# Optimization experiments

Hardware: AMD Instinct MI355X
Metric: run time of the kernel (lower is better)

The kernel has to match this reference:

```python
import jax, jax.numpy as jnp
import numpy as np

B, T, V, E, H = 2048, 80, 80, 8, 256  # batch, seq_len, vocab/num_classes, embed_dim, n_hidden
FORGET_BIAS = 1.0  # TF BasicLSTMCell default


def setup_inputs() -> dict:
    key = jax.random.key(0)
    ks = jax.random.split(key, 8)
    return {
        "features": jax.random.randint(ks[0], (B, T), 0, V, dtype=jnp.int32),
        "embedding": jax.random.normal(ks[1], (V, E), dtype=jnp.float32) * 0.1,
        "W1": jax.random.normal(ks[2], (E + H, 4 * H), dtype=jnp.float32) * 0.05,
        "b1": jnp.zeros((4 * H,), jnp.float32),
        "W2": jax.random.normal(ks[3], (H + H, 4 * H), dtype=jnp.float32) * 0.05,
        "b2": jnp.zeros((4 * H,), jnp.float32),
        "Wd": jax.random.normal(ks[4], (H, V), dtype=jnp.float32) * 0.05,
        "bd": jnp.zeros((V,), jnp.float32),
    }


def _lstm_layer(x, W, b):
    # x: [B, T, in]; TF BasicLSTMCell gate order: i, j(cell cand), f, o
    h_dim = W.shape[1] // 4

    def step(carry, xt):
        c, h = carry
        z = jnp.concatenate([xt, h], axis=-1) @ W + b  # [B, 4H]
        i, j, f, o = jnp.split(z, 4, axis=-1)
        c = c * jax.nn.sigmoid(f + FORGET_BIAS) + jax.nn.sigmoid(i) * jnp.tanh(j)
        h = jnp.tanh(c) * jax.nn.sigmoid(o)
        return (c, h), h

    b_dim = x.shape[0]
    init = (jnp.zeros((b_dim, h_dim), x.dtype), jnp.zeros((b_dim, h_dim), x.dtype))
    _, hs = jax.lax.scan(step, init, jnp.swapaxes(x, 0, 1))  # hs: [T, B, H]
    return jnp.swapaxes(hs, 0, 1)  # [B, T, H]


def reference(features, embedding, W1, b1, W2, b2, Wd, bd):
    x = embedding[features]            # [B, T, E] embedding lookup
    h1 = _lstm_layer(x, W1, b1)        # [B, T, H]
    h2 = _lstm_layer(h1, W2, b2)       # [B, T, H]
    logits = h2[:, -1, :] @ Wd + bd    # dense on last timestep -> [B, V]
    return logits
```

## Files before the change

### kernel.cpp

```cpp
#include <hip/hip_runtime.h>
#include <hip/hip_bf16.h>


#define BB 2048
#define TT 80
#define VV 80
#define HH 256

typedef _Float16 half8 __attribute__((ext_vector_type(8)));
typedef _Float16 half4v __attribute__((ext_vector_type(4)));
typedef float f32x4 __attribute__((ext_vector_type(4)));

__device__ __forceinline__ float sigf(float x) { return 1.0f / (1.0f + __expf(-x)); }
__device__ __forceinline__ float tanhfast(float x) { return 2.0f * sigf(2.0f * x) - 1.0f; }

__device__ __forceinline__ int swz(int row, int kbyte) {
    return row * 512 + (kbyte ^ ((row & 7) << 4));
}

__global__ void prep_table(const float* __restrict__ emb, const float* __restrict__ W1,
                           const float* __restrict__ b1, float* __restrict__ tbl) {
    int v = blockIdx.x, d = threadIdx.x;
    float4 s;
    s.x = b1[d]; s.y = b1[256 + d]; s.z = b1[512 + d] + 1.0f; s.w = b1[768 + d];
    #pragma unroll
    for (int e = 0; e < 8; ++e) {
        float xv = emb[v * 8 + e];
        const float* wr = W1 + (size_t)e * 1024;
        s.x = fmaf(xv, wr[d], s.x);
        s.y = fmaf(xv, wr[256 + d], s.y);
        s.z = fmaf(xv, wr[512 + d], s.z);
        s.w = fmaf(xv, wr[768 + d], s.w);
    }
    ((float4*)tbl)[v * 256 + d] = s;
}

__global__ void prep_w1_v2(const float* __restrict__ W1, _Float16* __restrict__ Wf) {
    int tid = blockIdx.x * 256 + threadIdx.x;
    int l = tid & 63, g = (tid >> 6) & 3, kk = (tid >> 8) & 7, w = (tid >> 11) & 15;
    int col = g * 256 + w * 16 + (l & 15);
    size_t base = ((size_t)((w * 8 + kk) * 4 + g) * 64 + l) * 8;
    #pragma unroll
    for (int e = 0; e < 8; ++e) {
        int krow = 8 + kk * 32 + (l >> 4) * 8 + e;
        Wf[base + e] = (_Float16)W1[(size_t)krow * 1024 + col];
    }
}
__global__ void prep_w2h_v2(const float* __restrict__ W2, _Float16* __restrict__ Wf) {
    int tid = blockIdx.x * 256 + threadIdx.x;
    int l = tid & 63, g = (tid >> 6) & 3, kk = (tid >> 8) & 7, w = (tid >> 11) & 15;
    int col = g * 256 + w * 16 + (l & 15);
    size_t base = ((size_t)((w * 8 + kk) * 4 + g) * 64 + l) * 8;
    #pragma unroll
    for (int e = 0; e < 8; ++e) {
        int krow = 256 + kk * 32 + (l >> 4) * 8 + e;
        Wf[base + e] = (_Float16)W2[(size_t)krow * 1024 + col];
    }
}
__global__ void prep_w2za_v2(const float* __restrict__ W2, _Float16* __restrict__ Wf) {
    int tid = blockIdx.x * 256 + threadIdx.x;
    int l = tid & 63, g = (tid >> 6) & 3, kk = (tid >> 8) & 7, w = (tid >> 11) & 15;
    int col = g * 256 + w * 16 + (l & 15);
    size_t base = ((size_t)((w * 8 + kk) * 4 + g) * 64 + l) * 8;
    #pragma unroll
    for (int e = 0; e < 8; ++e) {
        int krow = kk * 32 + (l >> 4) * 8 + e;
        Wf[base + e] = (_Float16)W2[(size_t)krow * 1024 + col];
    }
}
__global__ void prep_w2_old(const float* __restrict__ W2, _Float16* __restrict__ Wf) {
    int tid = blockIdx.x * 256 + threadIdx.x;
    int l = tid & 63, kk = (tid >> 6) & 7, j = (tid >> 9) & 1;
    int g = (tid >> 10) & 3, s = (tid >> 12) & 1, w = tid >> 13;
    int col = g * 256 + w * 32 + j * 16 + (l & 15);
    size_t base = ((size_t)((w * 16 + s * 8 + g * 2 + j) * 8 + kk) * 64 + l) * 8;
    #pragma unroll
    for (int e = 0; e < 8; ++e) {
        int krow = (1 - s) * 256 + kk * 32 + (l >> 4) * 8 + e;
        Wf[base + e] = (_Float16)W2[(size_t)krow * 1024 + col];
    }
}

__global__ __launch_bounds__(1024) void lstm1_v3(
    const int* __restrict__ feats, const float* __restrict__ tbl,
    const _Float16* __restrict__ Wf, _Float16* __restrict__ h1out)
{
    __shared__ char hb0[8192], hb1[8192];
    __shared__ int f_lds[16 * TT];
    const int tid = threadIdx.x, l = tid & 63, w = tid >> 6;
    const int row_a = l & 15, chunk = l >> 4;
    const int dim = w * 16 + (l & 15);
    const int crow0 = (l >> 4) * 4;
    const int brow = blockIdx.x * 16;

    for (int i = tid; i < 2048; i += 1024) ((float*)hb0)[i] = 0.f;
    for (int i = tid; i < 16 * TT; i += 1024)
        f_lds[i] = feats[(size_t)(brow + i / TT) * TT + (i % TT)];
    float c[4] = {};
    const float4* tblv = (const float4*)tbl;
    const half8* wp = (const half8*)Wf + (size_t)w * 2048;
    __syncthreads();

    for (int t = 0; t < TT; ++t) {
        char* cur = (t & 1) ? hb1 : hb0;
        char* nxt = (t & 1) ? hb0 : hb1;

        float4 tb[4];
        #pragma unroll
        for (int m = 0; m < 4; ++m) {
            int f = f_lds[(crow0 + m) * TT + t];
            tb[m] = tblv[f * 256 + dim];
        }

        f32x4 acc[4];
        #pragma unroll
        for (int g = 0; g < 4; ++g) acc[g] = (f32x4){0.f, 0.f, 0.f, 0.f};

        half8 wbuf[3][4];
        #pragma unroll
        for (int p = 0; p < 3; ++p)
            #pragma unroll
            for (int g = 0; g < 4; ++g) wbuf[p][g] = wp[(size_t)(p * 4 + g) * 64 + l];
        half8 aA = *(const half8*)(cur + swz(row_a, 0 * 64 + chunk * 16));
        half8 aB = *(const half8*)(cur + swz(row_a, 1 * 64 + chunk * 16));

        #pragma unroll
        for (int kk = 0; kk < 8; ++kk) {
            half8 av = (kk & 1) ? aB : aA;
            #pragma unroll
            for (int g = 0; g < 4; ++g)
                acc[g] = __builtin_amdgcn_mfma_f32_16x16x32_f16(
                    av, wbuf[kk % 3][g], acc[g], 0, 0, 0);
            if (kk + 2 < 8) {
                half8 an = *(const half8*)(cur + swz(row_a, (kk + 2) * 64 + chunk * 16));
                if (kk & 1) aB = an; else aA = an;
            }
            if (kk + 3 < 8) {
                #pragma unroll
                for (int g = 0; g < 4; ++g)
                    wbuf[(kk + 3) % 3][g] = wp[(size_t)((kk + 3) * 4 + g) * 64 + l];
            }
        }

        #pragma unroll
        for (int m = 0; m < 4; ++m) {
            const int R = crow0 + m;
            float zi = acc[0][m] + tb[m].x, zj = acc[1][m] + tb[m].y;
            float zf = acc[2][m] + tb[m].z, zo = acc[3][m] + tb[m].w;
            c[m] = c[m] * sigf(zf) + sigf(zi) * tanhfast(zj);
            float hv = tanhfast(c[m]) * sigf(zo);
            *(_Float16*)(nxt + swz(R, dim * 2)) = (_Float16)hv;
            h1out[((size_t)t * BB + brow + R) * HH + dim] = (_Float16)hv;
        }
        __syncthreads();
    }
}

__global__ __launch_bounds__(1024) void za_gemm_v3(
    const _Float16* __restrict__ h1, const _Float16* __restrict__ Wz,
    _Float16* __restrict__ za, int t0)
{
    const int tid = threadIdx.x, l = tid & 63, w = tid >> 6;
    const int chunk = l >> 4;
    const int dim = w * 16 + (l & 15);
    const size_t rloc = (size_t)blockIdx.x * 16;
    const size_t rglob = (size_t)t0 * BB + rloc;

    half8 a[8];
    #pragma unroll
    for (int kk = 0; kk < 8; ++kk)
        a[kk] = *(const half8*)(h1 + (rglob + (l & 15)) * HH + kk * 32 + chunk * 8);

    f32x4 acc[4];
    #pragma unroll
    for (int g = 0; g < 4; ++g) acc[g] = (f32x4){0.f, 0.f, 0.f, 0.f};
    const half8* wp = (const half8*)Wz + (size_t)w * 2048;
    half8 wbuf[2][4];
    #pragma unroll
    for (int g = 0; g < 4; ++g) wbuf[0][g] = wp[g * 64 + l];
    #pragma unroll
    for (int kk = 0; kk < 8; ++kk) {
        const int cur = kk & 1;
        if (kk < 7) {
            #pragma unroll
            for (int g = 0; g < 4; ++g)
                wbuf[cur ^ 1][g] = wp[(size_t)((kk + 1) * 4 + g) * 64 + l];
        }
        #pragma unroll
        for (int g = 0; g < 4; ++g)
            acc[g] = __builtin_amdgcn_mfma_f32_16x16x32_f16(
                a[kk], wbuf[cur][g], acc[g], 0, 0, 0);
    }
    #pragma unroll
    for (int m = 0; m < 4; ++m) {
        half4v v = { (_Float16)acc[0][m], (_Float16)acc[1][m],
                     (_Float16)acc[2][m], (_Float16)acc[3][m] };
        *(half4v*)(za + (rloc + chunk * 4 + m) * 1024 + dim * 4) = v;
    }
}

__global__ __launch_bounds__(1024) void lstm2_v3(
    const _Float16* __restrict__ za, const _Float16* __restrict__ Wf,
    const float* __restrict__ b2, float* __restrict__ c_state,
    _Float16* __restrict__ h_state, const float* __restrict__ Wd,
    const float* __restrict__ bd, float* __restrict__ out,
    int t0, int tc, int last)
{
    __shared__ char hb0[8192], hb1[8192];
    const int tid = threadIdx.x, l = tid & 63, w = tid >> 6;
    const int row_a = l & 15, chunk = l >> 4;
    const int dim = w * 16 + (l & 15);
    const int crow0 = (l >> 4) * 4;
    const int brow = blockIdx.x * 16;

    float bv[4];
    #pragma unroll
    for (int g = 0; g < 4; ++g) bv[g] = b2[g * 256 + dim] + (g == 2 ? 1.0f : 0.0f);

    float c[4];
    if (t0 == 0) {
        for (int i = tid; i < 2048; i += 1024) ((float*)hb0)[i] = 0.f;
        #pragma unroll
        for (int m = 0; m < 4; ++m) c[m] = 0.f;
    } else {
        for (int i = tid; i < 4096; i += 1024) {
            int r = i >> 8, d = i & 255;
            *(_Float16*)(hb0 + swz(r, d * 2)) = h_state[(size_t)(brow + r) * HH + d];
        }
        #pragma unroll
        for (int m = 0; m < 4; ++m)
            c[m] = c_state[(size_t)(brow + crow0 + m) * HH + dim];
    }
    const half8* wp = (const half8*)Wf + (size_t)w * 2048;
    __syncthreads();

    for (int tt = 0; tt < tc; ++tt) {
        char* cur = (tt & 1) ? hb1 : hb0;
        char* nxt = (tt & 1) ? hb0 : hb1;

        half4v zv[4];
        #pragma unroll
        for (int m = 0; m < 4; ++m)
            zv[m] = *(const half4v*)(za + ((size_t)tt * BB + brow + crow0 + m) * 1024 + dim * 4);

        f32x4 acc[4];
        #pragma unroll
        for (int g = 0; g < 4; ++g) acc[g] = (f32x4){0.f, 0.f, 0.f, 0.f};

        half8 wbuf[3][4];
        #pragma unroll
        for (int p = 0; p < 3; ++p)
            #pragma unroll
            for (int g = 0; g < 4; ++g) wbuf[p][g] = wp[(size_t)(p * 4 + g) * 64 + l];
        half8 aA = *(const half8*)(cur + swz(row_a, 0 * 64 + chunk * 16));
        half8 aB = *(const half8*)(cur + swz(row_a, 1 * 64 + chunk * 16));

        #pragma unroll
        for (int kk = 0; kk < 8; ++kk) {
            half8 av = (kk & 1) ? aB : aA;
            #pragma unroll
            for (int g = 0; g < 4; ++g)
                acc[g] = __builtin_amdgcn_mfma_f32_16x16x32_f16(
                    av, wbuf[kk % 3][g], acc[g], 0, 0, 0);
            if (kk + 2 < 8) {
                half8 an = *(const half8*)(cur + swz(row_a, (kk + 2) * 64 + chunk * 16));
                if (kk & 1) aB = an; else aA = an;
            }
            if (kk + 3 < 8) {
                #pragma unroll
                for (int g = 0; g < 4; ++g)
                    wbuf[(kk + 3) % 3][g] = wp[(size_t)((kk + 3) * 4 + g) * 64 + l];
            }
        }

        #pragma unroll
        for (int m = 0; m < 4; ++m) {
            const int R = crow0 + m;
            float zi = acc[0][m] + bv[0] + (float)zv[m][0];
            float zj = acc[1][m] + bv[1] + (float)zv[m][1];
            float zf = acc[2][m] + bv[2] + (float)zv[m][2];
            float zo = acc[3][m] + bv[3] + (float)zv[m][3];
            c[m] = c[m] * sigf(zf) + sigf(zi) * tanhfast(zj);
            float hv = tanhfast(c[m]) * sigf(zo);
            *(_Float16*)(nxt + swz(R, dim * 2)) = (_Float16)hv;
        }
        __syncthreads();
    }

    char* fin = (tc & 1) ? hb1 : hb0;
    if (!last) {
        #pragma unroll
        for (int m = 0; m < 4; ++m)
            c_state[(size_t)(brow + crow0 + m) * HH + dim] = c[m];
        for (int i = tid; i < 4096; i += 1024) {
            int r = i >> 8, d = i & 255;
            h_state[(size_t)(brow + r) * HH + d] = *(const _Float16*)(fin + swz(r, d * 2));
        }
    } else {
        for (int idx = tid; idx < 16 * VV; idx += 1024) {
            int r = idx / VV, v = idx - r * VV;
            float s = bd[v];
            for (int d = 0; d < HH; ++d)
                s = fmaf((float)*(const _Float16*)(fin + swz(r, d * 2)),
                         Wd[(size_t)d * VV + v], s);
            out[(size_t)(brow + r) * VV + v] = s;
        }
    }
}

__global__ __launch_bounds__(512, 2) void lstm2_old(
    const _Float16* __restrict__ h1, const _Float16* __restrict__ Wf,
    const float* __restrict__ b2, const float* __restrict__ Wd,
    const float* __restrict__ bd, float* __restrict__ out)
{
    __shared__ char h_lds[8192];
    const int tid = threadIdx.x, l = tid & 63, w = tid >> 6;
    const int brow = blockIdx.x * 16;
    const int row_a = l & 15, chunk = l >> 4;
    const int dim0 = w * 32 + (l & 15);

    for (int i = tid; i < 2048; i += 512) ((float*)h_lds)[i] = 0.f;
    float bv[2][4];
    #pragma unroll
    for (int j = 0; j < 2; ++j)
        #pragma unroll
        for (int g = 0; g < 4; ++g)
            bv[j][g] = b2[g * 256 + dim0 + j * 16] + (g == 2 ? 1.0f : 0.0f);
    float c[2][4] = {};
    __syncthreads();

    for (int t = 0; t < TT; ++t) {
        half8 a2[8];
        #pragma unroll
        for (int kk = 0; kk < 8; ++kk)
            a2[kk] = *(const half8*)(h_lds + swz(row_a, kk * 64 + chunk * 16));
        __syncthreads();

        half8 pa[8];
        const _Float16* hp = h1 + ((size_t)t * BB + brow + row_a) * HH + chunk * 8;
        #pragma unroll
        for (int kk = 0; kk < 8; ++kk) pa[kk] = *(const half8*)(hp + kk * 32);

        f32x4 acc[8];
        #pragma unroll
        for (int n = 0; n < 8; ++n) acc[n] = (f32x4){0.f, 0.f, 0.f, 0.f};
        const half8* wp = (const half8*)Wf + (size_t)w * 16 * 512;
        half8 wbuf[2][8];
        #pragma unroll
        for (int kk = 0; kk < 8; ++kk) wbuf[0][kk] = wp[(size_t)kk * 64 + l];
        #pragma unroll
        for (int gid = 0; gid < 16; ++gid) {
            const int cur = gid & 1;
            if (gid < 15) {
                #pragma unroll
                for (int kk = 0; kk < 8; ++kk)
                    wbuf[cur ^ 1][kk] = wp[(size_t)((gid + 1) * 8 + kk) * 64 + l];
            }
            const int s = gid >> 3, acci = gid & 7;
            #pragma unroll
            for (int kk = 0; kk < 8; ++kk)
                acc[acci] = __builtin_amdgcn_mfma_f32_16x16x32_f16(
                    s ? pa[kk] : a2[kk], wbuf[cur][kk], acc[acci], 0, 0, 0);
        }

        #pragma unroll
        for (int j = 0; j < 2; ++j) {
            const int D = dim0 + j * 16;
            #pragma unroll
            for (int m = 0; m < 4; ++m) {
                const int R = chunk * 4 + m;
                float zi = acc[j][m] + bv[j][0];
                float zj = acc[2 + j][m] + bv[j][1];
                float zf = acc[4 + j][m] + bv[j][2];
                float zo = acc[6 + j][m] + bv[j][3];
                c[j][m] = c[j][m] * sigf(zf) + sigf(zi) * tanhfast(zj);
                float hv = tanhfast(c[j][m]) * sigf(zo);
                *(_Float16*)(h_lds + swz(R, D * 2)) = (_Float16)hv;
            }
        }
        __syncthreads();
    }

    for (int idx = tid; idx < 16 * VV; idx += 512) {
        int r = idx / VV, v = idx - r * VV;
        float s = bd[v];
        for (int d = 0; d < HH; ++d) {
            float h2 = (float)*(const _Float16*)(h_lds + swz(r, d * 2));
            s = fmaf(h2, Wd[(size_t)d * VV + v], s);
        }
        out[(size_t)(brow + r) * VV + v] = s;
    }
}

extern "C" void kernel_launch(void* const* d_in, const int* in_sizes, int n_in,
                              void* d_out, int out_size, void* d_ws, size_t ws_size,
                              hipStream_t stream) {
    const int*   feats = (const int*)d_in[0];
    const float* emb   = (const float*)d_in[1];
    const float* W1    = (const float*)d_in[2];
    const float* b1    = (const float*)d_in[3];
    const float* W2    = (const float*)d_in[4];
    const float* b2    = (const float*)d_in[5];
    const float* Wd    = (const float*)d_in[6];
    const float* bd    = (const float*)d_in[7];
    float* out = (float*)d_out;

    char* ws = (char*)d_ws;
    float*    tbl     = (float*)ws;
    _Float16* W1f     = (_Float16*)(ws + (512u << 10));
    _Float16* W2h     = (_Float16*)(ws + (1024u << 10));
    _Float16* W2z     = (_Float16*)(ws + (1536u << 10));
    float*    c_state = (float*)(ws + (2u << 20));
    _Float16* h_state = (_Float16*)(ws + (4u << 20));
    _Float16* h1      = (_Float16*)(ws + (8u << 20));
    _Float16* za      = (_Float16*)(ws + (88u << 20));

    int TC = 0;
    if      (ws_size >= (160ull << 20)) TC = 16;
    else if (ws_size >= (128ull << 20)) TC = 8;
    else if (ws_size >= (108ull << 20)) TC = 4;

    prep_table<<<VV, 256, 0, stream>>>(emb, W1, b1, tbl);
    prep_w1_v2<<<128, 256, 0, stream>>>(W1, W1f);
    lstm1_v3<<<BB / 16, 1024, 0, stream>>>(feats, tbl, W1f, h1);

    if (TC) {
        prep_w2h_v2<<<128, 256, 0, stream>>>(W2, W2h);
        prep_w2za_v2<<<128, 256, 0, stream>>>(W2, W2z);
        for (int t0 = 0; t0 < TT; t0 += TC) {
            za_gemm_v3<<<(BB * TC) / 16, 1024, 0, stream>>>(h1, W2z, za, t0);
            lstm2_v3<<<BB / 16, 1024, 0, stream>>>(za, W2h, b2, c_state, h_state,
                                                   Wd, bd, out, t0, TC,
                                                   (t0 + TC == TT) ? 1 : 0);
        }
    } else {
        prep_w2_old<<<256, 256, 0, stream>>>(W2, W2h);
        lstm2_old<<<BB / 16, 512, 0, stream>>>(h1, W2h, b2, Wd, bd, out);
    }
}
```

Baseline: 2.006 ms.

## Retile LSTM recurrent kernels to 32 rows per block with 8 waves

```diff
diff --git a/kernel.cpp b/kernel.cpp
--- a/kernel.cpp
+++ b/kernel.cpp
@@ -35,22 +35,24 @@
     ((float4*)tbl)[v * 256 + d] = s;
 }
 
-__global__ void prep_w1_v2(const float* __restrict__ W1, _Float16* __restrict__ Wf) {
+__global__ void prep_w1_v6(const float* __restrict__ W1, _Float16* __restrict__ Wf) {
     int tid = blockIdx.x * 256 + threadIdx.x;
-    int l = tid & 63, g = (tid >> 6) & 3, kk = (tid >> 8) & 7, w = (tid >> 11) & 15;
-    int col = g * 256 + w * 16 + (l & 15);
-    size_t base = ((size_t)((w * 8 + kk) * 4 + g) * 64 + l) * 8;
+    int l = tid & 63, g = (tid >> 6) & 3, j = (tid >> 8) & 1;
+    int kk = (tid >> 9) & 7, w = (tid >> 12) & 7;
+    int col = g * 256 + w * 32 + j * 16 + (l & 15);
+    size_t base = ((size_t)((((w * 8 + kk) * 2 + j) * 4 + g)) * 64 + l) * 8;
     #pragma unroll
     for (int e = 0; e < 8; ++e) {
         int krow = 8 + kk * 32 + (l >> 4) * 8 + e;
         Wf[base + e] = (_Float16)W1[(size_t)krow * 1024 + col];
     }
 }
-__global__ void prep_w2h_v2(const float* __restrict__ W2, _Float16* __restrict__ Wf) {
+__global__ void prep_w2h_v6(const float* __restrict__ W2, _Float16* __restrict__ Wf) {
     int tid = blockIdx.x * 256 + threadIdx.x;
-    int l = tid & 63, g = (tid >> 6) & 3, kk = (tid >> 8) & 7, w = (tid >> 11) & 15;
-    int col = g * 256 + w * 16 + (l & 15);
-    size_t base = ((size_t)((w * 8 + kk) * 4 + g) * 64 + l) * 8;
+    int l = tid & 63, g = (tid >> 6) & 3, j = (tid >> 8) & 1;
+    int kk = (tid >> 9) & 7, w = (tid >> 12) & 7;
+    int col = g * 256 + w * 32 + j * 16 + (l & 15);
+    size_t base = ((size_t)((((w * 8 + kk) * 2 + j) * 4 + g)) * 64 + l) * 8;
     #pragma unroll
     for (int e = 0; e < 8; ++e) {
         int krow = 256 + kk * 32 + (l >> 4) * 8 + e;
@@ -81,78 +83,103 @@
     }
 }
 
-__global__ __launch_bounds__(1024) void lstm1_v3(
+__global__ __launch_bounds__(512, 2) void lstm1_v7(
     const int* __restrict__ feats, const float* __restrict__ tbl,
     const _Float16* __restrict__ Wf, _Float16* __restrict__ h1out)
 {
-    __shared__ char hb0[8192], hb1[8192];
-    __shared__ int f_lds[16 * TT];
+    __shared__ char hb0[16384], hb1[16384];
+    __shared__ int f_lds[32 * TT];
     const int tid = threadIdx.x, l = tid & 63, w = tid >> 6;
     const int row_a = l & 15, chunk = l >> 4;
-    const int dim = w * 16 + (l & 15);
+    const int dim0 = w * 32 + (l & 15);
     const int crow0 = (l >> 4) * 4;
-    const int brow = blockIdx.x * 16;
-
-    for (int i = tid; i < 2048; i += 1024) ((float*)hb0)[i] = 0.f;
-    for (int i = tid; i < 16 * TT; i += 1024)
+    const int brow = blockIdx.x * 32;
+
+    for (int i = tid; i < 4096; i += 512) ((float*)hb0)[i] = 0.f;
+    for (int i = tid; i < 32 * TT; i += 512)
         f_lds[i] = feats[(size_t)(brow + i / TT) * TT + (i % TT)];
-    float c[4] = {};
+    float c[2][2][4] = {};
     const float4* tblv = (const float4*)tbl;
-    const half8* wp = (const half8*)Wf + (size_t)w * 2048;
+    const half8* wp = (const half8*)Wf + (size_t)w * 4096;
+
+    half8 wbuf[2][8];
+    #pragma unroll
+    for (int jg = 0; jg < 8; ++jg) wbuf[0][jg] = wp[jg * 64 + l];
     __syncthreads();
 
     for (int t = 0; t < TT; ++t) {
         char* cur = (t & 1) ? hb1 : hb0;
         char* nxt = (t & 1) ? hb0 : hb1;
 
-        float4 tb[4];
-        #pragma unroll
-        for (int m = 0; m < 4; ++m) {
-            int f = f_lds[(crow0 + m) * TT + t];
-            tb[m] = tblv[f * 256 + dim];
-        }
-
-        f32x4 acc[4];
-        #pragma unroll
-        for (int g = 0; g < 4; ++g) acc[g] = (f32x4){0.f, 0.f, 0.f, 0.f};
-
-        half8 wbuf[3][4];
-        #pragma unroll
-        for (int p = 0; p < 3; ++p)
-            #pragma unroll
-            for (int g = 0; g < 4; ++g) wbuf[p][g] = wp[(size_t)(p * 4 + g) * 64 + l];
-        half8 aA = *(const half8*)(cur + swz(row_a, 0 * 64 + chunk * 16));
-        half8 aB = *(const half8*)(cur + swz(row_a, 1 * 64 + chunk * 16));
+        if (t > 0) {
+            #pragma unroll
+            for (int p = 0; p < 2; ++p) {
+                int i = p * 512 + tid, r = i >> 5, c16 = i & 31;
+                *(half8*)(h1out + ((size_t)(t - 1) * BB + brow + r) * HH + c16 * 8) =
+                    *(const half8*)(cur + swz(r, c16 * 16));
+            }
+        }
+
+        f32x4 acc[2][2][4];
+        #pragma unroll
+        for (int rt = 0; rt < 2; ++rt)
+            #pragma unroll
+            for (int j = 0; j < 2; ++j)
+                #pragma unroll
+                for (int g = 0; g < 4; ++g) acc[rt][j][g] = (f32x4){0.f, 0.f, 0.f, 0.f};
 
         #pragma unroll
         for (int kk = 0; kk < 8; ++kk) {
-            half8 av = (kk & 1) ? aB : aA;
-            #pragma unroll
-            for (int g = 0; g < 4; ++g)
-                acc[g] = __builtin_amdgcn_mfma_f32_16x16x32_f16(
-                    av, wbuf[kk % 3][g], acc[g], 0, 0, 0);
-            if (kk + 2 < 8) {
-                half8 an = *(const half8*)(cur + swz(row_a, (kk + 2) * 64 + chunk * 16));
-                if (kk & 1) aB = an; else aA = an;
+            const int cb = kk & 1;
+            const int ng = (kk + 1) & 7;
+            #pragma unroll
+            for (int jg = 0; jg < 8; ++jg)
+                wbuf[cb ^ 1][jg] = wp[(size_t)(ng * 8 + jg) * 64 + l];
+            half8 a0 = *(const half8*)(cur + swz(row_a,      kk * 64 + chunk * 16));
+            half8 a1 = *(const half8*)(cur + swz(row_a + 16, kk * 64 + chunk * 16));
+            #pragma unroll
+            for (int j = 0; j < 2; ++j)
+                #pragma unroll
+                for (int g = 0; g < 4; ++g) {
+                    acc[0][j][g] = __builtin_amdgcn_mfma_f32_16x16x32_f16(
+                        a0, wbuf[cb][j * 4 + g], acc[0][j][g], 0, 0, 0);
+                    acc[1][j][g] = __builtin_amdgcn_mfma_f32_16x16x32_f16(
+                        a1, wbuf[cb][j * 4 + g], acc[1][j][g], 0, 0, 0);
+                }
+        }
+
+        #pragma unroll
+        for (int rt = 0; rt < 2; ++rt) {
+            float4 tb[2][4];
+            #pragma unroll
+            for (int m = 0; m < 4; ++m) {
+                int f = f_lds[(rt * 16 + crow0 + m) * TT + t];
+                tb[0][m] = tblv[f * 256 + dim0];
+                tb[1][m] = tblv[f * 256 + dim0 + 16];
             }
-            if (kk + 3 < 8) {
-                #pragma unroll
-                for (int g = 0; g < 4; ++g)
-                    wbuf[(kk + 3) % 3][g] = wp[(size_t)((kk + 3) * 4 + g) * 64 + l];
-            }
-        }
-
-        #pragma unroll
-        for (int m = 0; m < 4; ++m) {
-            const int R = crow0 + m;
-            float zi = acc[0][m] + tb[m].x, zj = acc[1][m] + tb[m].y;
-            float zf = acc[2][m] + tb[m].z, zo = acc[3][m] + tb[m].w;
-            c[m] = c[m] * sigf(zf) + sigf(zi) * tanhfast(zj);
-            float hv = tanhfast(c[m]) * sigf(zo);
-            *(_Float16*)(nxt + swz(R, dim * 2)) = (_Float16)hv;
-            h1out[((size_t)t * BB + brow + R) * HH + dim] = (_Float16)hv;
+            #pragma unroll
+            for (int j = 0; j < 2; ++j)
+                #pragma unroll
+                for (int m = 0; m < 4; ++m) {
+                    float zi = acc[rt][j][0][m] + tb[j][m].x;
+                    float zj = acc[rt][j][1][m] + tb[j][m].y;
+                    float zf = acc[rt][j][2][m] + tb[j][m].z;
+                    float zo = acc[rt][j][3][m] + tb[j][m].w;
+                    float& cc = c[rt][j][m];
+                    cc = cc * sigf(zf) + sigf(zi) * tanhfast(zj);
+                    float hv = tanhfast(cc) * sigf(zo);
+                    *(_Float16*)(nxt + swz(rt * 16 + crow0 + m, (dim0 + j * 16) * 2)) =
+                        (_Float16)hv;
+                }
         }
         __syncthreads();
+    }
+
+    #pragma unroll
+    for (int p = 0; p < 2; ++p) {
+        int i = p * 512 + tid, r = i >> 5, c16 = i & 31;
+        *(half8*)(h1out + ((size_t)(TT - 1) * BB + brow + r) * HH + c16 * 8) =
+            *(const half8*)(hb0 + swz(r, c16 * 16));
     }
 }
 
@@ -199,90 +226,114 @@
     }
 }
 
-__global__ __launch_bounds__(1024) void lstm2_v3(
+__global__ __launch_bounds__(512, 2) void lstm2_v7(
     const _Float16* __restrict__ za, const _Float16* __restrict__ Wf,
     const float* __restrict__ b2, float* __restrict__ c_state,
     _Float16* __restrict__ h_state, const float* __restrict__ Wd,
     const float* __restrict__ bd, float* __restrict__ out,
     int t0, int tc, int last)
 {
-    __shared__ char hb0[8192], hb1[8192];
+    __shared__ char hb0[16384], hb1[16384];
     const int tid = threadIdx.x, l = tid & 63, w = tid >> 6;
     const int row_a = l & 15, chunk = l >> 4;
-    const int dim = w * 16 + (l & 15);
+    const int dim0 = w * 32 + (l & 15);
     const int crow0 = (l >> 4) * 4;
-    const int brow = blockIdx.x * 16;
-
-    float bv[4];
-    #pragma unroll
-    for (int g = 0; g < 4; ++g) bv[g] = b2[g * 256 + dim] + (g == 2 ? 1.0f : 0.0f);
-
-    float c[4];
+    const int brow = blockIdx.x * 32;
+
+    float bv[2][4];
+    #pragma unroll
+    for (int j = 0; j < 2; ++j)
+        #pragma unroll
+        for (int g = 0; g < 4; ++g)
+            bv[j][g] = b2[g * 256 + dim0 + j * 16] + (g == 2 ? 1.0f : 0.0f);
+
+    float c[2][2][4];
     if (t0 == 0) {
-        for (int i = tid; i < 2048; i += 1024) ((float*)hb0)[i] = 0.f;
-        #pragma unroll
-        for (int m = 0; m < 4; ++m) c[m] = 0.f;
+        for (int i = tid; i < 4096; i += 512) ((float*)hb0)[i] = 0.f;
+        #pragma unroll
+        for (int rt = 0; rt < 2; ++rt)
+            #pragma unroll
+            for (int j = 0; j < 2; ++j)
+                #pragma unroll
+                for (int m = 0; m < 4; ++m) c[rt][j][m] = 0.f;
     } else {
-        for (int i = tid; i < 4096; i += 1024) {
-            int r = i >> 8, d = i & 255;
-            *(_Float16*)(hb0 + swz(r, d * 2)) = h_state[(size_t)(brow + r) * HH + d];
-        }
-        #pragma unroll
-        for (int m = 0; m < 4; ++m)
-            c[m] = c_state[(size_t)(brow + crow0 + m) * HH + dim];
-    }
-    const half8* wp = (const half8*)Wf + (size_t)w * 2048;
+        #pragma unroll
+        for (int p = 0; p < 2; ++p) {
+            int i = p * 512 + tid, r = i >> 5, c16 = i & 31;
+            *(half8*)(hb0 + swz(r, c16 * 16)) =
+                *(const half8*)(h_state + (size_t)(brow + r) * HH + c16 * 8);
+        }
+        #pragma unroll
+        for (int rt = 0; rt < 2; ++rt)
+            #pragma unroll
+            for (int j = 0; j < 2; ++j)
+                #pragma unroll
+                for (int m = 0; m < 4; ++m)
+                    c[rt][j][m] = c_state[(size_t)(brow + rt * 16 + crow0 + m) * HH
+                                          + dim0 + j * 16];
+    }
+    const half8* wp = (const half8*)Wf + (size_t)w * 4096;
+    half8 wbuf[2][8];
+    #pragma unroll
+    for (int jg = 0; jg < 8; ++jg) wbuf[0][jg] = wp[jg * 64 + l];
     __syncthreads();
 
     for (int tt = 0; tt < tc; ++tt) {
         char* cur = (tt & 1) ? hb1 : hb0;
         char* nxt = (tt & 1) ? hb0 : hb1;
 
-        half4v zv[4];
-        #pragma unroll
-        for (int m = 0; m < 4; ++m)
-            zv[m] = *(const half4v*)(za + ((size_t)tt * BB + brow + crow0 + m) * 1024 + dim * 4);
-
-        f32x4 acc[4];
-        #pragma unroll
-        for (int g = 0; g < 4; ++g) acc[g] = (f32x4){0.f, 0.f, 0.f, 0.f};
-
-        half8 wbuf[3][4];
-        #pragma unroll
-        for (int p = 0; p < 3; ++p)
-            #pragma unroll
-            for (int g = 0; g < 4; ++g) wbuf[p][g] = wp[(size_t)(p * 4 + g) * 64 + l];
-        half8 aA = *(const half8*)(cur + swz(row_a, 0 * 64 + chunk * 16));
-        half8 aB = *(const half8*)(cur + swz(row_a, 1 * 64 + chunk * 16));
+        f32x4 acc[2][2][4];
+        #pragma unroll
+        for (int rt = 0; rt < 2; ++rt)
+            #pragma unroll
+            for (int j = 0; j < 2; ++j)
+                #pragma unroll
+                for (int g = 0; g < 4; ++g) acc[rt][j][g] = (f32x4){0.f, 0.f, 0.f, 0.f};
 
         #pragma unroll
         for (int kk = 0; kk < 8; ++kk) {
-            half8 av = (kk & 1) ? aB : aA;
-            #pragma unroll
-            for (int g = 0; g < 4; ++g)
-                acc[g] = __builtin_amdgcn_mfma_f32_16x16x32_f16(
-                    av, wbuf[kk % 3][g], acc[g], 0, 0, 0);
-            if (kk + 2 < 8) {
-                half8 an = *(const half8*)(cur + swz(row_a, (kk + 2) * 64 + chunk * 16));
-                if (kk & 1) aB = an; else aA = an;
-            }
-            if (kk + 3 < 8) {
-                #pragma unroll
-                for (int g = 0; g < 4; ++g)
-                    wbuf[(kk + 3) % 3][g] = wp[(size_t)((kk + 3) * 4 + g) * 64 + l];
-            }
-        }
-
-        #pragma unroll
-        for (int m = 0; m < 4; ++m) {
-            const int R = crow0 + m;
-            float zi = acc[0][m] + bv[0] + (float)zv[m][0];
-            float zj = acc[1][m] + bv[1] + (float)zv[m][1];
-            float zf = acc[2][m] + bv[2] + (float)zv[m][2];
-            float zo = acc[3][m] + bv[3] + (float)zv[m][3];
-            c[m] = c[m] * sigf(zf) + sigf(zi) * tanhfast(zj);
-            float hv = tanhfast(c[m]) * sigf(zo);
-            *(_Float16*)(nxt + swz(R, dim * 2)) = (_Float16)hv;
+            const int cb = kk & 1;
+            const int ng = (kk + 1) & 7;
+            #pragma unroll
+            for (int jg = 0; jg < 8; ++jg)
+                wbuf[cb ^ 1][jg] = wp[(size_t)(ng * 8 + jg) * 64 + l];
+            half8 a0 = *(const half8*)(cur + swz(row_a,      kk * 64 + chunk * 16));
+            half8 a1 = *(const half8*)(cur + swz(row_a + 16, kk * 64 + chunk * 16));
+            #pragma unroll
+            for (int j = 0; j < 2; ++j)
+                #pragma unroll
+                for (int g = 0; g < 4; ++g) {
+                    acc[0][j][g] = __builtin_amdgcn_mfma_f32_16x16x32_f16(
+                        a0, wbuf[cb][j * 4 + g], acc[0][j][g], 0, 0, 0);
+                    acc[1][j][g] = __builtin_amdgcn_mfma_f32_16x16x32_f16(
+                        a1, wbuf[cb][j * 4 + g], acc[1][j][g], 0, 0, 0);
+                }
+        }
+
+        #pragma unroll
+        for (int rt = 0; rt < 2; ++rt) {
+            half4v zv[2][4];
+            #pragma unroll
+            for (int j = 0; j < 2; ++j)
+                #pragma unroll
+                for (int m = 0; m < 4; ++m)
+                    zv[j][m] = *(const half4v*)(za +
+                        ((size_t)tt * BB + brow + rt * 16 + crow0 + m) * 1024
+                        + (dim0 + j * 16) * 4);
+            #pragma unroll
+            for (int j = 0; j < 2; ++j)
+                #pragma unroll
+                for (int m = 0; m < 4; ++m) {
+                    float zi = acc[rt][j][0][m] + bv[j][0] + (float)zv[j][m][0];
+                    float zj = acc[rt][j][1][m] + bv[j][1] + (float)zv[j][m][1];
+                    float zf = acc[rt][j][2][m] + bv[j][2] + (float)zv[j][m][2];
+                    float zo = acc[rt][j][3][m] + bv[j][3] + (float)zv[j][m][3];
+                    float& cc = c[rt][j][m];
+                    cc = cc * sigf(zf) + sigf(zi) * tanhfast(zj);
+                    float hv = tanhfast(cc) * sigf(zo);
+                    *(_Float16*)(nxt + swz(rt * 16 + crow0 + m, (dim0 + j * 16) * 2)) =
+                        (_Float16)hv;
+                }
         }
         __syncthreads();
     }
@@ -290,14 +341,21 @@
     char* fin = (tc & 1) ? hb1 : hb0;
     if (!last) {
         #pragma unroll
-        for (int m = 0; m < 4; ++m)
-            c_state[(size_t)(brow + crow0 + m) * HH + dim] = c[m];
-        for (int i = tid; i < 4096; i += 1024) {
-            int r = i >> 8, d = i & 255;
-            h_state[(size_t)(brow + r) * HH + d] = *(const _Float16*)(fin + swz(r, d * 2));
+        for (int rt = 0; rt < 2; ++rt)
+            #pragma unroll
+            for (int j = 0; j < 2; ++j)
+                #pragma unroll
+                for (int m = 0; m < 4; ++m)
+                    c_state[(size_t)(brow + rt * 16 + crow0 + m) * HH + dim0 + j * 16]
+                        = c[rt][j][m];
+        #pragma unroll
+        for (int p = 0; p < 2; ++p) {
+            int i = p * 512 + tid, r = i >> 5, c16 = i & 31;
+            *(half8*)(h_state + (size_t)(brow + r) * HH + c16 * 8) =
+                *(const half8*)(fin + swz(r, c16 * 16));
         }
     } else {
-        for (int idx = tid; idx < 16 * VV; idx += 1024) {
+        for (int idx = tid; idx < 32 * VV; idx += 512) {
             int r = idx / VV, v = idx - r * VV;
             float s = bd[v];
             for (int d = 0; d < HH; ++d)
@@ -421,17 +479,17 @@
     else if (ws_size >= (108ull << 20)) TC = 4;
 
     prep_table<<<VV, 256, 0, stream>>>(emb, W1, b1, tbl);
-    prep_w1_v2<<<128, 256, 0, stream>>>(W1, W1f);
-    lstm1_v3<<<BB / 16, 1024, 0, stream>>>(feats, tbl, W1f, h1);
+    prep_w1_v6<<<128, 256, 0, stream>>>(W1, W1f);
+    lstm1_v7<<<BB / 32, 512, 0, stream>>>(feats, tbl, W1f, h1);
 
     if (TC) {
-        prep_w2h_v2<<<128, 256, 0, stream>>>(W2, W2h);
+        prep_w2h_v6<<<128, 256, 0, stream>>>(W2, W2h);
         prep_w2za_v2<<<128, 256, 0, stream>>>(W2, W2z);
         for (int t0 = 0; t0 < TT; t0 += TC) {
             za_gemm_v3<<<(BB * TC) / 16, 1024, 0, stream>>>(h1, W2z, za, t0);
-            lstm2_v3<<<BB / 16, 1024, 0, stream>>>(za, W2h, b2, c_state, h_state,
-                                                   Wd, bd, out, t0, TC,
-                                                   (t0 + TC == TT) ? 1 : 0);
+            lstm2_v7<<<BB / 32, 512, 0, stream>>>(za, W2h, b2, c_state, h_state,
+                                                  Wd, bd, out, t0, TC,
+                                                  (t0 + TC == TT) ? 1 : 0);
         }
     } else {
         prep_w2_old<<<256, 256, 0, stream>>>(W2, W2h);
```

Result: slower. 3.196 ms (+59.3%).
